# Performance work log

Measured on AMD Instinct MI355X. Metric: run time of the kernel, lower is better.

Reference implementation:

```python
import jax, jax.numpy as jnp
import numpy as np

ALPHA = 0.2  # LeakyReLU negative slope
NHEADS = 3
N = 100000
DEG = 32
NFEAT = 256
NHID = 64
NCLASS = 40


def _gat_layer(x, dst, src, W, a_dst, a_src, concat):
    # SpGraphAttentionLayer: h = x @ W; e_ij = exp(-leakyrelu(a1.h_i + a2.h_j));
    # out_i = sum_j e_ij h_j / sum_j e_ij  (edge (i,j) has dst=i, src=j)
    n = x.shape[0]
    h = x @ W                                   # [N, F']
    logits = (h @ a_dst)[dst] + (h @ a_src)[src]  # [E]
    e = jnp.exp(-jax.nn.leaky_relu(logits, ALPHA))  # [E]
    denom = jax.ops.segment_sum(e, dst, num_segments=n)            # [N]
    num = jax.ops.segment_sum(e[:, None] * h[src], dst, num_segments=n)  # [N, F']
    out = num / (denom[:, None] + 1e-16)
    return jax.nn.elu(out) if concat else out


def setup_inputs() -> dict:
    key = jax.random.key(0)
    ks = jax.random.split(key, 8)
    x = jax.random.normal(ks[0], (N, NFEAT), dtype=jnp.float32)
    # random edges + self-loops so every node has at least one incoming edge
    rnd = jax.random.randint(ks[1], (2, N * DEG), 0, N, dtype=jnp.int64)
    loops = jnp.tile(jnp.arange(N, dtype=jnp.int64)[None, :], (2, 1))
    edge_index = jnp.concatenate([rnd, loops], axis=1)  # [2, E]
    s = 1.0 / np.sqrt(NFEAT)
    W = jax.random.uniform(ks[2], (NHEADS, NFEAT, NHID), jnp.float32, -s, s)
    a1 = jax.random.uniform(ks[3], (NHEADS, NHID), jnp.float32, -s, s)
    a2 = jax.random.uniform(ks[4], (NHEADS, NHID), jnp.float32, -s, s)
    s2 = 1.0 / np.sqrt(NHEADS * NHID)
    W_out = jax.random.uniform(ks[5], (NHEADS * NHID, NCLASS), jnp.float32, -s2, s2)
    a1_out = jax.random.uniform(ks[6], (NCLASS,), jnp.float32, -s2, s2)
    a2_out = jax.random.uniform(ks[7], (NCLASS,), jnp.float32, -s2, s2)
    return {"x": x, "edge_index": edge_index, "W": W, "a1": a1, "a2": a2,
            "W_out": W_out, "a1_out": a1_out, "a2_out": a2_out}


def reference(x, edge_index, W, a1, a2, W_out, a1_out, a2_out):
    # eval mode: dropout is identity
    dst, src = edge_index[0], edge_index[1]
    heads = [_gat_layer(x, dst, src, W[k], a1[k], a2[k], concat=True)
             for k in range(NHEADS)]
    h = jnp.concatenate(heads, axis=1)  # [N, NHEADS*NHID]
    out = _gat_layer(h, dst, src, W_out, a1_out, a2_out, concat=False)
    return jax.nn.elu(out)  # [N, NCLASS]
```

## Files before the change

### kernel.cpp

```cpp
#include <hip/hip_runtime.h>

#define ALPHA 0.2f
#define NFEAT 256
#define NHID 64
#define NHEADS 3
#define NCLASS 40

#define CSRB 256
#define LDSW 12512
#define NP8  (LDSW * 8)
#define NGRP 16

typedef short short8 __attribute__((ext_vector_type(8)));
typedef float float4v __attribute__((ext_vector_type(4)));
typedef _Float16 half4_t __attribute__((ext_vector_type(4)));

__device__ __forceinline__ float lrelu_negexp(float x) {
    float l = fmaxf(x, 0.f) + ALPHA * fminf(x, 0.f);
    return __expf(-l);
}
__device__ __forceinline__ float elu1(float x) {
    return x > 0.f ? x : (__expf(x) - 1.f);
}
__device__ __forceinline__ unsigned short f2bf(float f) {
    unsigned int u = __float_as_uint(f);
    unsigned int r = (u + 0x7FFFu + ((u >> 16) & 1u)) >> 16;
    return (unsigned short)r;
}
__device__ __forceinline__ float bf2f(unsigned short h) {
    return __uint_as_float(((unsigned int)h) << 16);
}
__device__ __forceinline__ float rdlane_f(float v, int l) {
    return __uint_as_float((unsigned)__builtin_amdgcn_readlane((int)__float_as_uint(v), l));
}

__global__ __launch_bounds__(256) void cvt_w_k(const float* __restrict__ W,
        unsigned short* __restrict__ wthi, unsigned short* __restrict__ wtlo) {
    int i = blockIdx.x * 256 + threadIdx.x;
    if (i >= NHEADS * NHID * NFEAT) return;
    int k = i & 255, nc = (i >> 8) & 63, head = i >> 14;
    float v = W[(size_t)head * NFEAT * NHID + (size_t)k * NHID + nc];
    unsigned short hi = f2bf(v);
    unsigned short lo = f2bf(v - bf2f(hi));
    wthi[i] = hi;
    wtlo[i] = lo;
}

__global__ __launch_bounds__(256) void gemm1_mfma_k(
        const float* __restrict__ x,
        const unsigned short* __restrict__ wthi, const unsigned short* __restrict__ wtlo,
        _Float16* __restrict__ h1h, int N) {
    __shared__ unsigned short Ah[128 * 40];
    __shared__ unsigned short Al[128 * 40];
    __shared__ unsigned short Bh[192 * 40];
    __shared__ unsigned short Bl[192 * 40];
    const int tid = threadIdx.x;
    const int wave = tid >> 6, lane = tid & 63;
    const int quad = lane >> 4, l16 = lane & 15;
    const int row0 = blockIdx.x * 128;
    const int wm = (wave >> 1) * 64;
    const int wn = (wave & 1) * 96;

    float4v acc[4][6];
#pragma unroll
    for (int s = 0; s < 4; ++s)
#pragma unroll
        for (int t = 0; t < 6; ++t)
            acc[s][t] = (float4v){0.f, 0.f, 0.f, 0.f};

    for (int kc = 0; kc < NFEAT; kc += 32) {
#pragma unroll
        for (int rr = 0; rr < 2; ++rr) {
            int idx = rr * 256 + tid;
            int r = idx >> 2, kq = (idx & 3) * 8;
            int gr = row0 + r; if (gr >= N) gr = N - 1;
            const float* xp = x + (size_t)gr * NFEAT + kc + kq;
            float4 f0 = *(const float4*)xp;
            float4 f1 = *(const float4*)(xp + 4);
            ushort4 h0, h1v, l0, l1;
            h0.x = f2bf(f0.x); l0.x = f2bf(f0.x - bf2f(h0.x));
            h0.y = f2bf(f0.y); l0.y = f2bf(f0.y - bf2f(h0.y));
            h0.z = f2bf(f0.z); l0.z = f2bf(f0.z - bf2f(h0.z));
            h0.w = f2bf(f0.w); l0.w = f2bf(f0.w - bf2f(h0.w));
            h1v.x = f2bf(f1.x); l1.x = f2bf(f1.x - bf2f(h1v.x));
            h1v.y = f2bf(f1.y); l1.y = f2bf(f1.y - bf2f(h1v.y));
            h1v.z = f2bf(f1.z); l1.z = f2bf(f1.z - bf2f(h1v.z));
            h1v.w = f2bf(f1.w); l1.w = f2bf(f1.w - bf2f(h1v.w));
            *(ushort4*)&Ah[r * 40 + kq]     = h0;
            *(ushort4*)&Ah[r * 40 + kq + 4] = h1v;
            *(ushort4*)&Al[r * 40 + kq]     = l0;
            *(ushort4*)&Al[r * 40 + kq + 4] = l1;
        }
#pragma unroll
        for (int rr = 0; rr < 3; ++rr) {
            int idx = rr * 256 + tid;
            int r = idx >> 2, kq = (idx & 3) * 8;
            size_t g = (size_t)r * NFEAT + kc + kq;
            *(int4*)&Bh[r * 40 + kq] = *(const int4*)(wthi + g);
            *(int4*)&Bl[r * 40 + kq] = *(const int4*)(wtlo + g);
        }
        __syncthreads();

        short8 ah[4], al[4];
#pragma unroll
        for (int s = 0; s < 4; ++s) {
            int m = wm + s * 16 + l16;
            ah[s] = *(const short8*)&Ah[m * 40 + quad * 8];
            al[s] = *(const short8*)&Al[m * 40 + quad * 8];
        }
#pragma unroll
        for (int t = 0; t < 6; ++t) {
            int n = wn + t * 16 + l16;
            short8 bh = *(const short8*)&Bh[n * 40 + quad * 8];
            short8 bl = *(const short8*)&Bl[n * 40 + quad * 8];
#pragma unroll
            for (int s = 0; s < 4; ++s) {
                acc[s][t] = __builtin_amdgcn_mfma_f32_16x16x32_bf16(ah[s], bh, acc[s][t], 0, 0, 0);
                acc[s][t] = __builtin_amdgcn_mfma_f32_16x16x32_bf16(ah[s], bl, acc[s][t], 0, 0, 0);
                acc[s][t] = __builtin_amdgcn_mfma_f32_16x16x32_bf16(al[s], bh, acc[s][t], 0, 0, 0);
            }
        }
        __syncthreads();
    }
#pragma unroll
    for (int s = 0; s < 4; ++s) {
#pragma unroll
        for (int r = 0; r < 4; ++r) {
            int grow = row0 + wm + s * 16 + quad * 4 + r;
            if (grow < N) {
#pragma unroll
                for (int t = 0; t < 6; ++t)
                    h1h[(size_t)grow * 192 + wn + t * 16 + l16] = (_Float16)acc[s][t][r];
            }
        }
    }
}

__global__ __launch_bounds__(256) void dots1_k(const _Float16* __restrict__ h1h,
        const float* __restrict__ a1, const float* __restrict__ a2,
        float* __restrict__ ad4, float* __restrict__ as4, int N) {
    int gt = blockIdx.x * 256 + threadIdx.x;
    int wid = gt >> 6, lane = gt & 63;
    if (wid >= N) return;
    const _Float16* hr = h1h + (size_t)wid * 192;
#pragma unroll
    for (int k = 0; k < 3; ++k) {
        float v = (float)hr[k*64 + lane];
        float da = v * a1[k*64 + lane];
        float db = v * a2[k*64 + lane];
#pragma unroll
        for (int o = 32; o > 0; o >>= 1) {
            da += __shfl_down(da, o, 64);
            db += __shfl_down(db, o, 64);
        }
        if (lane == 0) { ad4[wid*4+k] = da; as4[wid*4+k] = db; }
    }
}

__global__ __launch_bounds__(256) void hist_nib_k(const int* __restrict__ dst,
        unsigned* __restrict__ partial, int E) {
    __shared__ unsigned nib[LDSW];
    const int b = blockIdx.x, tid = threadIdx.x;
    for (int i = tid; i < LDSW; i += 256) nib[i] = 0u;
    __syncthreads();
    int chunk = (E + CSRB - 1) / CSRB;
    int e0 = b * chunk, e1 = min(E, e0 + chunk);
    for (int e = e0 + tid; e < e1; e += 256) {
        int d = dst[e];
        atomicAdd(&nib[d >> 3], 1u << ((d & 7) * 4));
    }
    __syncthreads();
    unsigned* p = partial + (size_t)b * LDSW;
    for (int i = tid; i < LDSW; i += 256) p[i] = nib[i];
}

__global__ __launch_bounds__(256) void bscan1_k(const unsigned* __restrict__ partial,
        unsigned char* __restrict__ prefix8, unsigned char* __restrict__ gsum8) {
    int t = blockIdx.x * 256 + threadIdx.x;
    if (t >= LDSW * NGRP) return;
    int g = t / LDSW, w = t - g * LDSW;
    unsigned run[8];
#pragma unroll
    for (int n = 0; n < 8; ++n) run[n] = 0u;
#pragma unroll
    for (int j = 0; j < 16; ++j) {
        int b = g * 16 + j;
        unsigned v = partial[(size_t)b * LDSW + w];
        unsigned lo = run[0] | (run[1] << 8) | (run[2] << 16) | (run[3] << 24);
        unsigned hi = run[4] | (run[5] << 8) | (run[6] << 16) | (run[7] << 24);
        *(uint2*)(prefix8 + (size_t)b * NP8 + (size_t)w * 8) = make_uint2(lo, hi);
#pragma unroll
        for (int n = 0; n < 8; ++n) run[n] += (v >> (n * 4)) & 15u;
    }
    unsigned lo = run[0] | (run[1] << 8) | (run[2] << 16) | (run[3] << 24);
    unsigned hi = run[4] | (run[5] << 8) | (run[6] << 16) | (run[7] << 24);
    *(uint2*)(gsum8 + (size_t)g * NP8 + (size_t)w * 8) = make_uint2(lo, hi);
}

__global__ __launch_bounds__(256) void bscan2_k(const unsigned char* __restrict__ gsum8,
        unsigned char* __restrict__ gpre8, int* __restrict__ cnt, int N) {
    int w = blockIdx.x * 256 + threadIdx.x;
    if (w >= LDSW) return;
    unsigned run[8];
#pragma unroll
    for (int n = 0; n < 8; ++n) run[n] = 0u;
#pragma unroll
    for (int g = 0; g < NGRP; ++g) {
        uint2 v = *(const uint2*)(gsum8 + (size_t)g * NP8 + (size_t)w * 8);
        unsigned lo = run[0] | (run[1] << 8) | (run[2] << 16) | (run[3] << 24);
        unsigned hi = run[4] | (run[5] << 8) | (run[6] << 16) | (run[7] << 24);
        *(uint2*)(gpre8 + (size_t)g * NP8 + (size_t)w * 8) = make_uint2(lo, hi);
        run[0] += v.x & 255u;         run[1] += (v.x >> 8) & 255u;
        run[2] += (v.x >> 16) & 255u; run[3] += (v.x >> 24) & 255u;
        run[4] += v.y & 255u;         run[5] += (v.y >> 8) & 255u;
        run[6] += (v.y >> 16) & 255u; run[7] += (v.y >> 24) & 255u;
    }
#pragma unroll
    for (int n = 0; n < 8; ++n) {
        int idx = w * 8 + n;
        if (idx < N) cnt[idx] = (int)run[n];
    }
}

__global__ __launch_bounds__(256) void scan1_k(const int* __restrict__ cnt,
        int* __restrict__ part, int* __restrict__ sums, int N) {
    __shared__ int s[256];
    int tid = threadIdx.x, b = blockIdx.x;
    int base = b * 2048 + tid * 8;
    int v[8]; int t = 0;
#pragma unroll
    for (int i = 0; i < 8; ++i) { int idx = base + i; v[i] = (idx < N) ? cnt[idx] : 0; t += v[i]; }
    s[tid] = t; __syncthreads();
    for (int o = 1; o < 256; o <<= 1) {
        int u = (tid >= o) ? s[tid - o] : 0;
        __syncthreads();
        s[tid] += u;
        __syncthreads();
    }
    int run = s[tid] - t;
#pragma unroll
    for (int i = 0; i < 8; ++i) { int idx = base + i; if (idx < N) part[idx] = run; run += v[i]; }
    if (tid == 255) sums[b] = s[255];
}

__global__ void scan2_k(int* sums, int nb) {
    if (threadIdx.x == 0 && blockIdx.x == 0) {
        int run = 0;
        for (int i = 0; i < nb; ++i) { int t = sums[i]; sums[i] = run; run += t; }
    }
}

__global__ __launch_bounds__(256) void scan3_k(const int* __restrict__ part,
        const int* __restrict__ sums, int* __restrict__ ptr, int N, int E) {
    int i = blockIdx.x * 256 + threadIdx.x;
    if (i < N) ptr[i] = part[i] + sums[i >> 11];
    if (i == 0) ptr[N] = E;
}

__global__ __launch_bounds__(256) void scatter_nib_k(const int* __restrict__ dst,
        const int* __restrict__ src, const int* __restrict__ ptr,
        const unsigned char* __restrict__ prefix8, const unsigned char* __restrict__ gpre8,
        int* __restrict__ csr, int E) {
    __shared__ unsigned nib[LDSW];
    const int b = blockIdx.x, tid = threadIdx.x;
    for (int i = tid; i < LDSW; i += 256) nib[i] = 0u;
    __syncthreads();
    const unsigned char* pb = prefix8 + (size_t)b * NP8;
    const unsigned char* gp = gpre8 + (size_t)(b >> 4) * NP8;
    int chunk = (E + CSRB - 1) / CSRB;
    int e0 = b * chunk, e1 = min(E, e0 + chunk);
    for (int e = e0 + tid; e < e1; e += 256) {
        int d = dst[e];
        unsigned old = atomicAdd(&nib[d >> 3], 1u << ((d & 7) * 4));
        int local = (int)((old >> ((d & 7) * 4)) & 15u);
        csr[ptr[d] + (int)gp[d] + (int)pb[d] + local] = src[e];
    }
}

__global__ __launch_bounds__(256) void agg1f_k(const _Float16* __restrict__ h1h,
        const float4* __restrict__ ad4, const float4* __restrict__ as4,
        const int* __restrict__ ptr, const int* __restrict__ csr,
        _Float16* __restrict__ out1h, int N) {
    int gt = blockIdx.x * 256 + threadIdx.x;
    int wid = gt >> 6, lane = gt & 63;
    if (wid >= N) return;
    int p0 = __builtin_amdgcn_readfirstlane(ptr[wid]);
    int p1 = __builtin_amdgcn_readfirstlane(ptr[wid + 1]);
    float4 ad = ad4[wid];
    const _Float16* hb = h1h + lane;
    float acc0 = 0.f, acc1 = 0.f, acc2 = 0.f;
    float dx = 0.f, dy = 0.f, dz = 0.f;

    for (int b0 = p0; b0 < p1; b0 += 64) {
        int e = b0 + lane;
        int cnt = min(64, p1 - b0);
        int si = 0; float wx = 0.f, wy = 0.f, wz = 0.f;
        if (e < p1) {
            si = csr[e];
            float4 as = as4[si];
            wx = lrelu_negexp(ad.x + as.x);
            wy = lrelu_negexp(ad.y + as.y);
            wz = lrelu_negexp(ad.z + as.z);
            dx += wx; dy += wy; dz += wz;
        }
        int jn = cnt & ~7;
        for (int j = 0; j < jn; j += 8) {
            float va[8], vb[8], vc[8], wxr[8], wyr[8], wzr[8];
#pragma unroll
            for (int i = 0; i < 8; ++i) {
                int s = __builtin_amdgcn_readlane(si, j + i);
                wxr[i] = rdlane_f(wx, j + i);
                wyr[i] = rdlane_f(wy, j + i);
                wzr[i] = rdlane_f(wz, j + i);
                const _Float16* hp = hb + (size_t)s * 192;
                va[i] = (float)hp[0];
                vb[i] = (float)hp[64];
                vc[i] = (float)hp[128];
            }
#pragma unroll
            for (int i = 0; i < 8; ++i) {
                acc0 = fmaf(wxr[i], va[i], acc0);
                acc1 = fmaf(wyr[i], vb[i], acc1);
                acc2 = fmaf(wzr[i], vc[i], acc2);
            }
        }
        for (int j = jn; j < cnt; ++j) {
            int s = __builtin_amdgcn_readlane(si, j);
            float wxx = rdlane_f(wx, j), wyy = rdlane_f(wy, j), wzz = rdlane_f(wz, j);
            const _Float16* hp = hb + (size_t)s * 192;
            acc0 = fmaf(wxx, (float)hp[0], acc0);
            acc1 = fmaf(wyy, (float)hp[64], acc1);
            acc2 = fmaf(wzz, (float)hp[128], acc2);
        }
    }

#pragma unroll
    for (int o = 32; o > 0; o >>= 1) {
        dx += __shfl_xor(dx, o, 64);
        dy += __shfl_xor(dy, o, 64);
        dz += __shfl_xor(dz, o, 64);
    }
    size_t ob = (size_t)wid * 192;
    out1h[ob + lane]       = (_Float16)elu1(acc0 / (dx + 1e-16f));
    out1h[ob + 64 + lane]  = (_Float16)elu1(acc1 / (dy + 1e-16f));
    out1h[ob + 128 + lane] = (_Float16)elu1(acc2 / (dz + 1e-16f));
}

__global__ __launch_bounds__(256) void gemm2_k(const _Float16* __restrict__ X,
        const float* __restrict__ Wo, const float* __restrict__ a1o,
        const float* __restrict__ a2o, _Float16* __restrict__ h2h,
        float* __restrict__ ad2, float* __restrict__ as2, int N) {
    __shared__ float Xs[32][193];
    __shared__ float Ws[192 * 40];
    const int tid = threadIdx.x;
    const int row0 = blockIdx.x * 32;
    for (int i = tid; i < 192 * 40; i += 256) Ws[i] = Wo[i];
    for (int i = tid; i < 32 * 48; i += 256) {
        int r = i / 48, c4 = (i % 48) * 4;
        int rr = row0 + r; if (rr >= N) rr = N - 1;
        half4_t v = *(const half4_t*)(X + (size_t)rr * 192 + c4);
        Xs[r][c4+0] = (float)v.x; Xs[r][c4+1] = (float)v.y;
        Xs[r][c4+2] = (float)v.z; Xs[r][c4+3] = (float)v.w;
    }
    __syncthreads();
    int rsub = tid >> 3;
    int f0 = (tid & 7) * 5;
    float acc[5] = {0, 0, 0, 0, 0};
    for (int c = 0; c < 192; ++c) {
        float xv = Xs[rsub][c];
#pragma unroll
        for (int j = 0; j < 5; ++j) acc[j] = fmaf(xv, Ws[c*40 + f0 + j], acc[j]);
    }
    int r = row0 + rsub;
    if (r < N) {
        float da = 0.f, db = 0.f;
#pragma unroll
        for (int j = 0; j < 5; ++j) {
            h2h[(size_t)r*64 + f0 + j] = (_Float16)acc[j];
            float hv = (float)(_Float16)acc[j];
            da = fmaf(hv, a1o[f0 + j], da);
            db = fmaf(hv, a2o[f0 + j], db);
        }
#pragma unroll
        for (int o = 4; o > 0; o >>= 1) {
            da += __shfl_down(da, o, 8);
            db += __shfl_down(db, o, 8);
        }
        if ((tid & 7) == 0) { ad2[r] = da; as2[r] = db; }
    }
}

__global__ __launch_bounds__(256) void agg2f_k(const _Float16* __restrict__ h2h,
        const float* __restrict__ ad2, const float* __restrict__ as2,
        const int* __restrict__ ptr, const int* __restrict__ csr,
        float* __restrict__ out, int N) {
    int gt = blockIdx.x * 256 + threadIdx.x;
    int wid = gt >> 6, lane = gt & 63;
    if (wid >= N) return;
    int p0 = __builtin_amdgcn_readfirstlane(ptr[wid]);
    int p1 = __builtin_amdgcn_readfirstlane(ptr[wid + 1]);
    float ad = ad2[wid];
    const _Float16* hb = h2h + lane;
    float acc = 0.f, den = 0.f;

    for (int b0 = p0; b0 < p1; b0 += 64) {
        int e = b0 + lane;
        int cnt = min(64, p1 - b0);
        int si = 0; float w = 0.f;
        if (e < p1) {
            si = csr[e];
            w = lrelu_negexp(ad + as2[si]);
            den += w;
        }
        int jn = cnt & ~15;
        for (int j = 0; j < jn; j += 16) {
            float v[16], cw[16];
#pragma unroll
            for (int i = 0; i < 16; ++i) {
                int s = __builtin_amdgcn_readlane(si, j + i);
                cw[i] = rdlane_f(w, j + i);
                v[i] = (float)hb[(size_t)s * 64];
            }
#pragma unroll
            for (int i = 0; i < 16; ++i) acc = fmaf(cw[i], v[i], acc);
        }
        for (int j = jn; j < cnt; ++j) {
            int s = __builtin_amdgcn_readlane(si, j);
            float cw = rdlane_f(w, j);
            acc = fmaf(cw, (float)hb[(size_t)s * 64], acc);
        }
    }

#pragma unroll
    for (int o = 32; o > 0; o >>= 1) den += __shfl_xor(den, o, 64);
    if (lane < 40) {
        out[(size_t)wid * 40 + lane] = elu1(acc / (den + 1e-16f));
    }
}

extern "C" void kernel_launch(void* const* d_in, const int* in_sizes, int n_in,
                              void* d_out, int out_size, void* d_ws, size_t ws_size,
                              hipStream_t stream) {
    const float* x   = (const float*)d_in[0];
    const int*   ei  = (const int*)d_in[1];
    const float* W   = (const float*)d_in[2];
    const float* a1  = (const float*)d_in[3];
    const float* a2  = (const float*)d_in[4];
    const float* Wo  = (const float*)d_in[5];
    const float* a1o = (const float*)d_in[6];
    const float* a2o = (const float*)d_in[7];
    const int N = in_sizes[0] / NFEAT;
    const int E = in_sizes[1] / 2;
    const int* dst = ei;
    const int* src = ei + E;

    char* base = (char*)d_ws;
    size_t off = 0;
    auto alloc = [&](size_t bytes) { void* p = base + off; off += (bytes + 255) & ~(size_t)255; return p; };
    _Float16* h1h   = (_Float16*)alloc((size_t)N * 192 * 2);
    _Float16* out1h = (_Float16*)alloc((size_t)N * 192 * 2);
    int*      csr   = (int*)alloc((size_t)E * 4);
    unsigned* partial = (unsigned*)alloc((size_t)CSRB * LDSW * 4);
    unsigned char* prefix8 = (unsigned char*)alloc((size_t)CSRB * NP8);
    unsigned char* gsum8   = (unsigned char*)alloc((size_t)NGRP * NP8);
    unsigned char* gpre8   = (unsigned char*)alloc((size_t)NGRP * NP8);
    char*     bufA  = (char*)alloc((size_t)N * 144 + 4096);
    int*      ptr   = (int*)alloc((size_t)(N + 1) * 4);
    int*      cnt   = (int*)alloc((size_t)N * 4);
    int*      part  = (int*)alloc((size_t)N * 4);
    int*      sums  = (int*)alloc(1024);
    float*    ad4   = (float*)alloc((size_t)N * 4 * 4);
    float*    as4   = (float*)alloc((size_t)N * 4 * 4);
    unsigned short* wthi = (unsigned short*)alloc((size_t)NHEADS * NHID * NFEAT * 2);
    unsigned short* wtlo = (unsigned short*)alloc((size_t)NHEADS * NHID * NFEAT * 2);

    _Float16* h2h = (_Float16*)bufA;
    float*    ad2 = (float*)(bufA + (size_t)N * 128 + 1024);
    float*    as2 = ad2 + N;

    cvt_w_k<<<(NHEADS * NHID * NFEAT + 255) / 256, 256, 0, stream>>>(W, wthi, wtlo);
    gemm1_mfma_k<<<(N + 127) / 128, 256, 0, stream>>>(x, wthi, wtlo, h1h, N);

    hist_nib_k<<<CSRB, 256, 0, stream>>>(dst, partial, E);
    bscan1_k<<<(LDSW * NGRP + 255) / 256, 256, 0, stream>>>(partial, prefix8, gsum8);
    bscan2_k<<<(LDSW + 255) / 256, 256, 0, stream>>>(gsum8, gpre8, cnt, N);
    int nb = (N + 2047) / 2048;
    scan1_k<<<nb, 256, 0, stream>>>(cnt, part, sums, N);
    scan2_k<<<1, 64, 0, stream>>>(sums, nb);
    scan3_k<<<(N + 255) / 256, 256, 0, stream>>>(part, sums, ptr, N, E);
    scatter_nib_k<<<CSRB, 256, 0, stream>>>(dst, src, ptr, prefix8, gpre8, csr, E);

    dots1_k<<<(N + 3) / 4, 256, 0, stream>>>(h1h, a1, a2, ad4, as4, N);
    agg1f_k<<<(N + 3) / 4, 256, 0, stream>>>(h1h, (const float4*)ad4,
                                             (const float4*)as4, ptr, csr, out1h, N);

    gemm2_k<<<(N + 31) / 32, 256, 0, stream>>>(out1h, Wo, a1o, a2o, h2h, ad2, as2, N);
    agg2f_k<<<(N + 3) / 4, 256, 0, stream>>>(h2h, ad2, as2, ptr, csr, (float*)d_out, N);
}
```

Measured before the change: 791.9 us.

## Fuse attention dot products into GEMM1 epilogue and merge degree scan kernels

Computes the per-head a1/a2 dot products inside the GEMM1 epilogue from the fp16-rounded accumulators. It reduces them with lane shuffles plus a small LDS buffer, which removes the separate dots1 kernel that re-read h1h. It also folds the bscan2 pass into the first scan stage, dropping the cnt buffer and one launch, and replaces the serial single-thread block-sum scan with a wave shuffle scan. The cost is extra registers and LDS work in the GEMM epilogue; the shuffle scan assumes there are at most 64 blocks.

```diff
diff --git a/kernel.cpp b/kernel.cpp
--- a/kernel.cpp
+++ b/kernel.cpp
@@ -49,7 +49,9 @@
 __global__ __launch_bounds__(256) void gemm1_mfma_k(
         const float* __restrict__ x,
         const unsigned short* __restrict__ wthi, const unsigned short* __restrict__ wtlo,
-        _Float16* __restrict__ h1h, int N) {
+        const float* __restrict__ a1, const float* __restrict__ a2,
+        _Float16* __restrict__ h1h, float* __restrict__ ad4, float* __restrict__ as4,
+        int N) {
     __shared__ unsigned short Ah[128 * 40];
     __shared__ unsigned short Al[128 * 40];
     __shared__ unsigned short Bh[192 * 40];
@@ -122,38 +124,64 @@
         }
         __syncthreads();
     }
+
+    float* red = (float*)Ah;
+    for (int i = tid; i < 1536; i += 256) red[i] = 0.f;
+    __syncthreads();
+
+    float a1v[6], a2v[6];
+#pragma unroll
+    for (int t = 0; t < 6; ++t) {
+        int c = wn + t * 16 + l16;
+        a1v[t] = a1[c];
+        a2v[t] = a2[c];
+    }
+    const int half = wave & 1;
+    const int tsplit = half ? 2 : 4;
+    const int headA = half ? 1 : 0;
+    const int headB = headA + 1;
+
 #pragma unroll
     for (int s = 0; s < 4; ++s) {
 #pragma unroll
         for (int r = 0; r < 4; ++r) {
-            int grow = row0 + wm + s * 16 + quad * 4 + r;
-            if (grow < N) {
-#pragma unroll
-                for (int t = 0; t < 6; ++t)
-                    h1h[(size_t)grow * 192 + wn + t * 16 + l16] = (_Float16)acc[s][t][r];
-            }
-        }
-    }
-}
-
-__global__ __launch_bounds__(256) void dots1_k(const _Float16* __restrict__ h1h,
-        const float* __restrict__ a1, const float* __restrict__ a2,
-        float* __restrict__ ad4, float* __restrict__ as4, int N) {
-    int gt = blockIdx.x * 256 + threadIdx.x;
-    int wid = gt >> 6, lane = gt & 63;
-    if (wid >= N) return;
-    const _Float16* hr = h1h + (size_t)wid * 192;
-#pragma unroll
-    for (int k = 0; k < 3; ++k) {
-        float v = (float)hr[k*64 + lane];
-        float da = v * a1[k*64 + lane];
-        float db = v * a2[k*64 + lane];
-#pragma unroll
-        for (int o = 32; o > 0; o >>= 1) {
-            da += __shfl_down(da, o, 64);
-            db += __shfl_down(db, o, 64);
-        }
-        if (lane == 0) { ad4[wid*4+k] = da; as4[wid*4+k] = db; }
+            int row = wm + s * 16 + quad * 4 + r;
+            int grow = row0 + row;
+            float dA = 0.f, dB = 0.f, sA = 0.f, sB = 0.f;
+#pragma unroll
+            for (int t = 0; t < 6; ++t) {
+                _Float16 hq = (_Float16)acc[s][t][r];
+                if (grow < N)
+                    h1h[(size_t)grow * 192 + wn + t * 16 + l16] = hq;
+                float hv = (float)hq;
+                if (t < tsplit) { dA = fmaf(hv, a1v[t], dA); sA = fmaf(hv, a2v[t], sA); }
+                else            { dB = fmaf(hv, a1v[t], dB); sB = fmaf(hv, a2v[t], sB); }
+            }
+#pragma unroll
+            for (int m = 1; m < 16; m <<= 1) {
+                dA += __shfl_xor(dA, m, 64);
+                dB += __shfl_xor(dB, m, 64);
+                sA += __shfl_xor(sA, m, 64);
+                sB += __shfl_xor(sB, m, 64);
+            }
+            if (l16 == 0) {
+                red[(headA * 2 + half) * 128 + row] = dA;
+                red[(headB * 2 + half) * 128 + row] = dB;
+                red[768 + (headA * 2 + half) * 128 + row] = sA;
+                red[768 + (headB * 2 + half) * 128 + row] = sB;
+            }
+        }
+    }
+    __syncthreads();
+    for (int i = tid; i < 128; i += 256) {
+        int grow = row0 + i;
+        if (grow < N) {
+#pragma unroll
+            for (int h = 0; h < 3; ++h) {
+                ad4[grow * 4 + h] = red[(h * 2) * 128 + i] + red[(h * 2 + 1) * 128 + i];
+                as4[grow * 4 + h] = red[768 + (h * 2) * 128 + i] + red[768 + (h * 2 + 1) * 128 + i];
+            }
+        }
     }
 }
 
@@ -197,39 +225,31 @@
     *(uint2*)(gsum8 + (size_t)g * NP8 + (size_t)w * 8) = make_uint2(lo, hi);
 }
 
-__global__ __launch_bounds__(256) void bscan2_k(const unsigned char* __restrict__ gsum8,
-        unsigned char* __restrict__ gpre8, int* __restrict__ cnt, int N) {
-    int w = blockIdx.x * 256 + threadIdx.x;
-    if (w >= LDSW) return;
-    unsigned run[8];
-#pragma unroll
-    for (int n = 0; n < 8; ++n) run[n] = 0u;
-#pragma unroll
-    for (int g = 0; g < NGRP; ++g) {
-        uint2 v = *(const uint2*)(gsum8 + (size_t)g * NP8 + (size_t)w * 8);
-        unsigned lo = run[0] | (run[1] << 8) | (run[2] << 16) | (run[3] << 24);
-        unsigned hi = run[4] | (run[5] << 8) | (run[6] << 16) | (run[7] << 24);
-        *(uint2*)(gpre8 + (size_t)g * NP8 + (size_t)w * 8) = make_uint2(lo, hi);
-        run[0] += v.x & 255u;         run[1] += (v.x >> 8) & 255u;
-        run[2] += (v.x >> 16) & 255u; run[3] += (v.x >> 24) & 255u;
-        run[4] += v.y & 255u;         run[5] += (v.y >> 8) & 255u;
-        run[6] += (v.y >> 16) & 255u; run[7] += (v.y >> 24) & 255u;
-    }
-#pragma unroll
-    for (int n = 0; n < 8; ++n) {
-        int idx = w * 8 + n;
-        if (idx < N) cnt[idx] = (int)run[n];
-    }
-}
-
-__global__ __launch_bounds__(256) void scan1_k(const int* __restrict__ cnt,
-        int* __restrict__ part, int* __restrict__ sums, int N) {
+__global__ __launch_bounds__(256) void bscan2s_k(const unsigned char* __restrict__ gsum8,
+        unsigned char* __restrict__ gpre8, int* __restrict__ part,
+        int* __restrict__ sums, int N) {
     __shared__ int s[256];
     int tid = threadIdx.x, b = blockIdx.x;
-    int base = b * 2048 + tid * 8;
-    int v[8]; int t = 0;
-#pragma unroll
-    for (int i = 0; i < 8; ++i) { int idx = base + i; v[i] = (idx < N) ? cnt[idx] : 0; t += v[i]; }
+    int w = b * 256 + tid;
+    unsigned run[8];
+#pragma unroll
+    for (int n = 0; n < 8; ++n) run[n] = 0u;
+    if (w < LDSW) {
+#pragma unroll
+        for (int g = 0; g < NGRP; ++g) {
+            uint2 v = *(const uint2*)(gsum8 + (size_t)g * NP8 + (size_t)w * 8);
+            unsigned lo = run[0] | (run[1] << 8) | (run[2] << 16) | (run[3] << 24);
+            unsigned hi = run[4] | (run[5] << 8) | (run[6] << 16) | (run[7] << 24);
+            *(uint2*)(gpre8 + (size_t)g * NP8 + (size_t)w * 8) = make_uint2(lo, hi);
+            run[0] += v.x & 255u;         run[1] += (v.x >> 8) & 255u;
+            run[2] += (v.x >> 16) & 255u; run[3] += (v.x >> 24) & 255u;
+            run[4] += v.y & 255u;         run[5] += (v.y >> 8) & 255u;
+            run[6] += (v.y >> 16) & 255u; run[7] += (v.y >> 24) & 255u;
+        }
+    }
+    int t = 0;
+#pragma unroll
+    for (int n = 0; n < 8; ++n) t += (int)run[n];
     s[tid] = t; __syncthreads();
     for (int o = 1; o < 256; o <<= 1) {
         int u = (tid >= o) ? s[tid - o] : 0;
@@ -237,17 +257,26 @@
         s[tid] += u;
         __syncthreads();
     }
-    int run = s[tid] - t;
-#pragma unroll
-    for (int i = 0; i < 8; ++i) { int idx = base + i; if (idx < N) part[idx] = run; run += v[i]; }
+    int runp = s[tid] - t;
+#pragma unroll
+    for (int n = 0; n < 8; ++n) {
+        int idx = w * 8 + n;
+        if (idx < N) part[idx] = runp;
+        runp += (int)run[n];
+    }
     if (tid == 255) sums[b] = s[255];
 }
 
 __global__ void scan2_k(int* sums, int nb) {
-    if (threadIdx.x == 0 && blockIdx.x == 0) {
-        int run = 0;
-        for (int i = 0; i < nb; ++i) { int t = sums[i]; sums[i] = run; run += t; }
-    }
+    int tid = threadIdx.x;
+    int v = (tid < nb) ? sums[tid] : 0;
+    int run = v;
+#pragma unroll
+    for (int o = 1; o < 64; o <<= 1) {
+        int u = __shfl_up(run, o, 64);
+        if (tid >= o) run += u;
+    }
+    if (tid < nb) sums[tid] = run - v;
 }
 
 __global__ __launch_bounds__(256) void scan3_k(const int* __restrict__ part,
@@ -466,7 +495,6 @@
     unsigned char* gpre8   = (unsigned char*)alloc((size_t)NGRP * NP8);
     char*     bufA  = (char*)alloc((size_t)N * 144 + 4096);
     int*      ptr   = (int*)alloc((size_t)(N + 1) * 4);
-    int*      cnt   = (int*)alloc((size_t)N * 4);
     int*      part  = (int*)alloc((size_t)N * 4);
     int*      sums  = (int*)alloc(1024);
     float*    ad4   = (float*)alloc((size_t)N * 4 * 4);
@@ -479,18 +507,17 @@
     float*    as2 = ad2 + N;
 
     cvt_w_k<<<(NHEADS * NHID * NFEAT + 255) / 256, 256, 0, stream>>>(W, wthi, wtlo);
-    gemm1_mfma_k<<<(N + 127) / 128, 256, 0, stream>>>(x, wthi, wtlo, h1h, N);
+    gemm1_mfma_k<<<(N + 127) / 128, 256, 0, stream>>>(x, wthi, wtlo, a1, a2,
+                                                      h1h, ad4, as4, N);
 
     hist_nib_k<<<CSRB, 256, 0, stream>>>(dst, partial, E);
     bscan1_k<<<(LDSW * NGRP + 255) / 256, 256, 0, stream>>>(partial, prefix8, gsum8);
-    bscan2_k<<<(LDSW + 255) / 256, 256, 0, stream>>>(gsum8, gpre8, cnt, N);
-    int nb = (N + 2047) / 2048;
-    scan1_k<<<nb, 256, 0, stream>>>(cnt, part, sums, N);
-    scan2_k<<<1, 64, 0, stream>>>(sums, nb);
+    int nb2 = (LDSW + 255) / 256;
+    bscan2s_k<<<nb2, 256, 0, stream>>>(gsum8, gpre8, part, sums, N);
+    scan2_k<<<1, 64, 0, stream>>>(sums, nb2);
     scan3_k<<<(N + 255) / 256, 256, 0, stream>>>(part, sums, ptr, N, E);
     scatter_nib_k<<<CSRB, 256, 0, stream>>>(dst, src, ptr, prefix8, gpre8, csr, E);
 
-    dots1_k<<<(N + 3) / 4, 256, 0, stream>>>(h1h, a1, a2, ad4, as4, N);
     agg1f_k<<<(N + 3) / 4, 256, 0, stream>>>(h1h, (const float4*)ad4,
                                              (const float4*)as4, ptr, csr, out1h, N);
 
```

New measurement: 768.1 us. 3.0% less time.
